# Kernel optimization log

Hardware: AMD Instinct MI355X
Metric: run time of the kernel (lower is better)

Reference implementation:

```python
import jax, jax.numpy as jnp
import numpy as np

N = 2_000_000
C = 64
BS = 8
MAX_LEN = 256_000


def setup_inputs() -> dict:
    key = jax.random.key(0)
    k1, k2 = jax.random.split(key)
    inds = jax.random.randint(k1, (N, 4), 0, BS, dtype=jnp.int32)
    features = jax.random.normal(k2, (N, C), dtype=jnp.float32)
    return {"inds": inds, "features": features, "bs": BS, "max_length": MAX_LEN}


def reference(inds, features, bs, max_length):
    # Scatter ragged per-batch features into a zero-padded dense [bs, max_length, C] tensor.
    b = inds[:, 0]                                  # [N] batch id per point
    n = b.shape[0]
    # bincount of batch ids (fixed length bs)
    counts = jnp.zeros((bs,), jnp.int32).at[b].add(1)
    starts = jnp.cumsum(counts) - counts            # start offset of each batch group
    # stable sort by batch id gives within-group rank = global rank - group start
    perm = jnp.argsort(b)                           # jnp.argsort is stable
    pos_sorted = jnp.arange(n, dtype=jnp.int32) - starts[b[perm]]
    pos = jnp.zeros((n,), jnp.int32).at[perm].set(pos_sorted)  # within-batch slot per point
    out = jnp.zeros((bs, max_length, features.shape[-1]), features.dtype)
    out = out.at[b, pos].set(features)
    return out
```

## Files before the change

### kernel.cpp

```cpp
#include <hip/hip_runtime.h>

#define BLOCK  256
#define ITEMS  16
#define CHUNK  (BLOCK * ITEMS)
#define NBATCH 8
#define MAXLEN 256000
#define CROW4  16

__global__ __launch_bounds__(BLOCK) void hist_kernel(const int4* __restrict__ inds,
                                                     int n,
                                                     int* __restrict__ blockCounts) {
    int base = blockIdx.x * CHUNK;
    __shared__ int cnt[NBATCH];
    if (threadIdx.x < NBATCH) cnt[threadIdx.x] = 0;
    __syncthreads();

    unsigned long long p8 = 0;
#pragma unroll
    for (int k = 0; k < ITEMS; ++k) {
        int idx = base + k * BLOCK + threadIdx.x;
        if (idx < n) {
            int b = inds[idx].x;
            p8 += 1ull << (8 * b);
        }
    }
    unsigned long long lo = 0, hi = 0;
#pragma unroll
    for (int j = 0; j < 4; ++j) {
        lo |= ((p8 >> (8 * j)) & 0xFFull) << (16 * j);
        hi |= ((p8 >> (8 * (j + 4))) & 0xFFull) << (16 * j);
    }
#pragma unroll
    for (int d = 1; d < 64; d <<= 1) {
        lo += __shfl_xor(lo, d, 64);
        hi += __shfl_xor(hi, d, 64);
    }
    int lane = threadIdx.x & 63;
    if (lane == 0) {
#pragma unroll
        for (int j = 0; j < 4; ++j) {
            atomicAdd(&cnt[j],     (int)((lo >> (16 * j)) & 0xFFFFull));
            atomicAdd(&cnt[j + 4], (int)((hi >> (16 * j)) & 0xFFFFull));
        }
    }
    __syncthreads();
    if (threadIdx.x < NBATCH)
        blockCounts[blockIdx.x * NBATCH + threadIdx.x] = cnt[threadIdx.x];
}

__global__ __launch_bounds__(512) void scan_kernel(const int* __restrict__ blockCounts,
                                                   int numBlocks,
                                                   int* __restrict__ blockOffsets,
                                                   int* __restrict__ totals) {
    int w = threadIdx.x >> 6;
    int lane = threadIdx.x & 63;
    int carry = 0;
    for (int c = 0; c < numBlocks; c += 64) {
        int i = c + lane;
        int v = (i < numBlocks) ? blockCounts[i * NBATCH + w] : 0;
        int x = v;
#pragma unroll
        for (int d = 1; d < 64; d <<= 1) {
            int y = __shfl_up(x, d, 64);
            if (lane >= d) x += y;
        }
        if (i < numBlocks) blockOffsets[i * NBATCH + w] = carry + x - v;
        carry += __shfl(x, 63, 64);
    }
    if (lane == 0) totals[w] = carry;
}

__global__ __launch_bounds__(BLOCK) void zero_tail_kernel(float4* __restrict__ out,
                                                          const int* __restrict__ totals) {
    int b = blockIdx.y;
    int cnt = totals[b];
    if (cnt > MAXLEN) cnt = MAXLEN;
    int start = (b * MAXLEN + cnt) * CROW4;
    int end   = (b + 1) * MAXLEN * CROW4;
    float4 z = make_float4(0.f, 0.f, 0.f, 0.f);
    for (int i = start + blockIdx.x * BLOCK + threadIdx.x; i < end; i += gridDim.x * BLOCK)
        out[i] = z;
}

__global__ __launch_bounds__(BLOCK) void scatter_kernel(const int4*  __restrict__ inds,
                                                        const float4* __restrict__ feat,
                                                        const int*   __restrict__ blockOffsets,
                                                        float4* __restrict__ out,
                                                        int n) {
    __shared__ int bsh[CHUNK];
    __shared__ int dsh[CHUNK];
    __shared__ int off[BLOCK * 9];
    __shared__ int boff[NBATCH];
    __shared__ unsigned long long wlo[4], whi[4];

    int tid = threadIdx.x;
    int base = blockIdx.x * CHUNK;
    if (tid < NBATCH) boff[tid] = blockOffsets[blockIdx.x * NBATCH + tid];

#pragma unroll
    for (int k = 0; k < ITEMS; ++k) {
        int idx = base + k * BLOCK + tid;
        bsh[k * BLOCK + tid] = (idx < n) ? inds[idx].x : -1;
    }
    __syncthreads();

    int s = tid * ITEMS;
    unsigned long long p8 = 0;
#pragma unroll
    for (int j = 0; j < ITEMS; ++j) {
        int b = bsh[s + j];
        if (b >= 0) p8 += 1ull << (8 * b);
    }
    unsigned long long lo = 0, hi = 0;
#pragma unroll
    for (int j = 0; j < 4; ++j) {
        lo |= ((p8 >> (8 * j)) & 0xFFull) << (16 * j);
        hi |= ((p8 >> (8 * (j + 4))) & 0xFFull) << (16 * j);
    }

    unsigned long long slo = lo, shi = hi;
    int lane = tid & 63, wave = tid >> 6;
#pragma unroll
    for (int d = 1; d < 64; d <<= 1) {
        unsigned long long tlo = __shfl_up(slo, d, 64);
        unsigned long long thi = __shfl_up(shi, d, 64);
        if (lane >= d) { slo += tlo; shi += thi; }
    }
    if (lane == 63) { wlo[wave] = slo; whi[wave] = shi; }
    __syncthreads();
    unsigned long long plo = slo - lo, phi = shi - hi;
#pragma unroll
    for (int w = 0; w < 4; ++w)
        if (w < wave) { plo += wlo[w]; phi += whi[w]; }

#pragma unroll
    for (int j = 0; j < 4; ++j) {
        off[tid * 9 + j]     = boff[j]     + (int)((plo >> (16 * j)) & 0xFFFF);
        off[tid * 9 + j + 4] = boff[j + 4] + (int)((phi >> (16 * j)) & 0xFFFF);
    }

#pragma unroll
    for (int j = 0; j < ITEMS; ++j) {
        int e = s + j;
        int b = bsh[e];
        if (b >= 0) {
            int r = off[tid * 9 + b]++;
            dsh[e] = (r < MAXLEN) ? (b * MAXLEN + r) : -1;
        } else {
            dsh[e] = -1;
        }
    }
    __syncthreads();

    int lane16 = tid & 15;
    int rg = tid >> 4;
    for (int r0 = 0; r0 < CHUNK; r0 += 16) {
        int e = r0 + rg;
        int dst = dsh[e];
        if (dst >= 0) {
            int src = base + e;
            out[dst * CROW4 + lane16] = feat[src * CROW4 + lane16];
        }
    }
}

extern "C" void kernel_launch(void* const* d_in, const int* in_sizes, int n_in,
                              void* d_out, int out_size, void* d_ws, size_t ws_size,
                              hipStream_t stream) {
    const int4*   inds = (const int4*)d_in[0];
    const float4* feat = (const float4*)d_in[1];
    float4* out = (float4*)d_out;
    int n = in_sizes[0] / 4;
    int numBlocks = (n + CHUNK - 1) / CHUNK;

    int* blockCounts  = (int*)d_ws;
    int* blockOffsets = blockCounts + numBlocks * NBATCH;
    int* totals       = blockOffsets + numBlocks * NBATCH;

    hist_kernel<<<numBlocks, BLOCK, 0, stream>>>(inds, n, blockCounts);
    scan_kernel<<<1, 512, 0, stream>>>(blockCounts, numBlocks, blockOffsets, totals);
    zero_tail_kernel<<<dim3(64, NBATCH), BLOCK, 0, stream>>>(out, totals);
    scatter_kernel<<<numBlocks, BLOCK, 0, stream>>>(inds, feat, blockOffsets, out, n);
}
```

Baseline: 894.3 us.

## Compact batch ids to bytes, fuse tail zeroing into scatter, pad shared index array

The histogram pass now also writes each point's batch id as one byte into workspace, so the scatter pass reads 16 ids per thread with a single int4 load instead of re-reading the strided int4 index array. The separate tail-zeroing kernel is folded into the end of the scatter kernel, which drops a launch. The shared destination array is padded to avoid bank conflicts, the copy loop issues two row loads before their stores, and launch bounds now request 6 waves for occupancy. The risk is that the byte array is written at unbounded idx for the last block, which relies on workspace slack and on the totals pointer's alignment for the int4 reads.

```diff
diff --git a/kernel.cpp b/kernel.cpp
--- a/kernel.cpp
+++ b/kernel.cpp
@@ -7,9 +7,13 @@
 #define MAXLEN 256000
 #define CROW4  16
 
+#define DSHI(e) ((e) + ((e) >> 4))
+#define DSHSZ   (CHUNK + CHUNK / 16)
+
 __global__ __launch_bounds__(BLOCK) void hist_kernel(const int4* __restrict__ inds,
                                                      int n,
-                                                     int* __restrict__ blockCounts) {
+                                                     int* __restrict__ blockCounts,
+                                                     unsigned char* __restrict__ bcomp) {
     int base = blockIdx.x * CHUNK;
     __shared__ int cnt[NBATCH];
     if (threadIdx.x < NBATCH) cnt[threadIdx.x] = 0;
@@ -19,10 +23,12 @@
 #pragma unroll
     for (int k = 0; k < ITEMS; ++k) {
         int idx = base + k * BLOCK + threadIdx.x;
+        int b = 0xFF;
         if (idx < n) {
-            int b = inds[idx].x;
+            b = inds[idx].x;
             p8 += 1ull << (8 * b);
         }
+        bcomp[idx] = (unsigned char)b;
     }
     unsigned long long lo = 0, hi = 0;
 #pragma unroll
@@ -70,25 +76,12 @@
     if (lane == 0) totals[w] = carry;
 }
 
-__global__ __launch_bounds__(BLOCK) void zero_tail_kernel(float4* __restrict__ out,
-                                                          const int* __restrict__ totals) {
-    int b = blockIdx.y;
-    int cnt = totals[b];
-    if (cnt > MAXLEN) cnt = MAXLEN;
-    int start = (b * MAXLEN + cnt) * CROW4;
-    int end   = (b + 1) * MAXLEN * CROW4;
-    float4 z = make_float4(0.f, 0.f, 0.f, 0.f);
-    for (int i = start + blockIdx.x * BLOCK + threadIdx.x; i < end; i += gridDim.x * BLOCK)
-        out[i] = z;
-}
-
-__global__ __launch_bounds__(BLOCK) void scatter_kernel(const int4*  __restrict__ inds,
-                                                        const float4* __restrict__ feat,
-                                                        const int*   __restrict__ blockOffsets,
-                                                        float4* __restrict__ out,
-                                                        int n) {
-    __shared__ int bsh[CHUNK];
-    __shared__ int dsh[CHUNK];
+__global__ __launch_bounds__(BLOCK, 6) void scatter_kernel(const int4*  __restrict__ bcomp4,
+                                                           const float4* __restrict__ feat,
+                                                           const int*   __restrict__ blockOffsets,
+                                                           const int*   __restrict__ totals,
+                                                           float4* __restrict__ out) {
+    __shared__ int dsh[DSHSZ];
     __shared__ int off[BLOCK * 9];
     __shared__ int boff[NBATCH];
     __shared__ unsigned long long wlo[4], whi[4];
@@ -97,19 +90,19 @@
     int base = blockIdx.x * CHUNK;
     if (tid < NBATCH) boff[tid] = blockOffsets[blockIdx.x * NBATCH + tid];
 
-#pragma unroll
-    for (int k = 0; k < ITEMS; ++k) {
-        int idx = base + k * BLOCK + tid;
-        bsh[k * BLOCK + tid] = (idx < n) ? inds[idx].x : -1;
-    }
-    __syncthreads();
+    int4 bv = bcomp4[blockIdx.x * BLOCK + tid];
+    unsigned int w0 = (unsigned int)bv.x, w1 = (unsigned int)bv.y;
+    unsigned int w2 = (unsigned int)bv.z, w3 = (unsigned int)bv.w;
 
-    int s = tid * ITEMS;
     unsigned long long p8 = 0;
 #pragma unroll
-    for (int j = 0; j < ITEMS; ++j) {
-        int b = bsh[s + j];
-        if (b >= 0) p8 += 1ull << (8 * b);
+    for (int q = 0; q < 4; ++q) {
+        unsigned int w = (q == 0) ? w0 : (q == 1) ? w1 : (q == 2) ? w2 : w3;
+#pragma unroll
+        for (int j = 0; j < 4; ++j) {
+            int b = (int)((w >> (8 * j)) & 0xFF);
+            if (b != 0xFF) p8 += 1ull << (8 * b);
+        }
     }
     unsigned long long lo = 0, hi = 0;
 #pragma unroll
@@ -139,28 +132,46 @@
         off[tid * 9 + j + 4] = boff[j + 4] + (int)((phi >> (16 * j)) & 0xFFFF);
     }
 
+    int s = tid * ITEMS;
 #pragma unroll
-    for (int j = 0; j < ITEMS; ++j) {
-        int e = s + j;
-        int b = bsh[e];
-        if (b >= 0) {
-            int r = off[tid * 9 + b]++;
-            dsh[e] = (r < MAXLEN) ? (b * MAXLEN + r) : -1;
-        } else {
-            dsh[e] = -1;
+    for (int q = 0; q < 4; ++q) {
+        unsigned int w = (q == 0) ? w0 : (q == 1) ? w1 : (q == 2) ? w2 : w3;
+#pragma unroll
+        for (int j = 0; j < 4; ++j) {
+            int e = s + 4 * q + j;
+            int b = (int)((w >> (8 * j)) & 0xFF);
+            if (b != 0xFF) {
+                int r = off[tid * 9 + b]++;
+                dsh[DSHI(e)] = (r < MAXLEN) ? (b * MAXLEN + r) : -1;
+            } else {
+                dsh[DSHI(e)] = -1;
+            }
         }
     }
     __syncthreads();
 
     int lane16 = tid & 15;
     int rg = tid >> 4;
-    for (int r0 = 0; r0 < CHUNK; r0 += 16) {
-        int e = r0 + rg;
-        int dst = dsh[e];
-        if (dst >= 0) {
-            int src = base + e;
-            out[dst * CROW4 + lane16] = feat[src * CROW4 + lane16];
-        }
+    for (int r0 = 0; r0 < CHUNK; r0 += 32) {
+        int e0 = r0 + rg, e1 = e0 + 16;
+        int d0 = dsh[DSHI(e0)], d1 = dsh[DSHI(e1)];
+        bool p0 = (d0 >= 0), p1 = (d1 >= 0);
+        float4 v0, v1;
+        if (p0) v0 = feat[(base + e0) * CROW4 + lane16];
+        if (p1) v1 = feat[(base + e1) * CROW4 + lane16];
+        if (p0) out[d0 * CROW4 + lane16] = v0;
+        if (p1) out[d1 * CROW4 + lane16] = v1;
+    }
+
+    float4 z = make_float4(0.f, 0.f, 0.f, 0.f);
+#pragma unroll
+    for (int b = 0; b < NBATCH; ++b) {
+        int cnt = totals[b];
+        if (cnt > MAXLEN) cnt = MAXLEN;
+        int s4 = (b * MAXLEN + cnt) * CROW4;
+        int e4 = (b + 1) * MAXLEN * CROW4;
+        for (int i = s4 + blockIdx.x * BLOCK + tid; i < e4; i += gridDim.x * BLOCK)
+            out[i] = z;
     }
 }
 
@@ -176,9 +187,10 @@
     int* blockCounts  = (int*)d_ws;
     int* blockOffsets = blockCounts + numBlocks * NBATCH;
     int* totals       = blockOffsets + numBlocks * NBATCH;
+    unsigned char* bcomp = (unsigned char*)(totals + NBATCH);
 
-    hist_kernel<<<numBlocks, BLOCK, 0, stream>>>(inds, n, blockCounts);
+    hist_kernel<<<numBlocks, BLOCK, 0, stream>>>(inds, n, blockCounts, bcomp);
     scan_kernel<<<1, 512, 0, stream>>>(blockCounts, numBlocks, blockOffsets, totals);
-    zero_tail_kernel<<<dim3(64, NBATCH), BLOCK, 0, stream>>>(out, totals);
-    scatter_kernel<<<numBlocks, BLOCK, 0, stream>>>(inds, feat, blockOffsets, out, n);
+    scatter_kernel<<<numBlocks, BLOCK, 0, stream>>>((const int4*)bcomp, feat,
+                                                    blockOffsets, totals, out);
 }
```

After: 960.4 us. 7.4% more time.
